# Kernel tuning notes

Hardware: AMD Instinct MI355X
Metric: run time of the kernel (lower is better)

Reference implementation:

```python
import jax, jax.numpy as jnp
import numpy as np

# Dims: B=4, C_in=256, H=W=64 -> L=4096, token_dim D=256, state_dim N=512, K=4
B_, C_IN, H_, W_ = 4, 256, 64, 64
D, N, K = 256, 512, 4


def setup_inputs() -> dict:
    key = jax.random.key(0)
    ks = jax.random.split(key, 16)
    g = lambda k, shape, sc=0.02: (jax.random.normal(k, shape, jnp.float32) * sc)
    return {
        'feat_map': jax.random.normal(ks[0], (B_, C_IN, H_, W_), jnp.float32),
        'hf_map':   jax.random.normal(ks[1], (B_, C_IN, H_, W_), jnp.float32),
        # 1x1 conv proj_f / proj_hf: weight (out=D, in=C_IN), bias (D,)
        'Wf':  g(ks[2], (D, C_IN)), 'bf':  jnp.zeros((D,), jnp.float32),
        'Whf': g(ks[3], (D, C_IN)), 'bhf': jnp.zeros((D,), jnp.float32),
        # alpha_head: Linear(D, D//2) -> GELU -> Linear(D//2, K)
        'Wa1': g(ks[4], (D // 2, D)), 'ba1': jnp.zeros((D // 2,), jnp.float32),
        'Wa2': g(ks[5], (K, D // 2)), 'ba2': jnp.zeros((K,), jnp.float32),
        # SelectiveSSM base tuples: diagonal decay logits A (K,N), input maps B (K,N,D), output maps C (K,D,N)
        'A_base': g(ks[6], (K, N), 1.0),
        'B_base': g(ks[7], (K, N, D), 0.02),
        'C_base': g(ks[8], (K, D, N), 0.02),
        # out_proj 1x1 conv: (C_IN, D)
        'Wout': g(ks[9], (C_IN, D)), 'bout': jnp.zeros((C_IN,), jnp.float32),
    }


def _stage(feat_map, hf_map, Wf, bf, Whf, bhf, Wa1, ba1, Wa2, ba2,
           A_base, B_base, C_base, Wout, bout):
    B, C, H, W = feat_map.shape
    L = H * W
    # 1x1 conv token projections -> (B, L, D)
    t_f = jnp.einsum('bchw,dc->bdhw', feat_map, Wf) + bf[None, :, None, None]
    t_hf = jnp.einsum('bchw,dc->bdhw', hf_map, Whf) + bhf[None, :, None, None]
    x = t_f.reshape(B, -1, L).transpose(0, 2, 1)        # (B, L, D)
    t_hf_seq = t_hf.reshape(B, -1, L).transpose(0, 2, 1)  # (B, L, D)
    # gating MLP -> per-token mixture weights over K base SSMs
    hmid = jax.nn.gelu(t_hf_seq @ Wa1.T + ba1, approximate=False)
    alpha = jax.nn.softmax(hmid @ Wa2.T + ba2, axis=-1)  # (B, L, K)
    # selective SSM: per-token mixed diagonal decay and input drive
    a = jax.nn.sigmoid(jnp.einsum('blk,kn->bln', alpha, A_base))   # (B, L, N)
    u = jnp.einsum('bld,blk,knd->bln', x, alpha, B_base)           # (B, L, N)

    def step(h, au):
        a_t, u_t = au                   # each (B, N)
        h = a_t * h + u_t
        return h, h

    h0 = jnp.zeros((B, a.shape[-1]), x.dtype)
    _, hs = jax.lax.scan(step, h0, (a.transpose(1, 0, 2), u.transpose(1, 0, 2)))
    h_seq = hs.transpose(1, 0, 2)                                   # (B, L, N)
    # mixed readout
    y = jnp.einsum('blk,bln,kdn->bld', alpha, h_seq, C_base)        # (B, L, D)
    y_map = y.transpose(0, 2, 1).reshape(B, -1, H, W)
    out = jnp.einsum('bdhw,cd->bchw', y_map, Wout) + bout[None, :, None, None]
    return out


def reference(feat_map, hf_map, Wf, bf, Whf, bhf, Wa1, ba1, Wa2, ba2,
              A_base, B_base, C_base, Wout, bout):
    return _stage(feat_map, hf_map, Wf, bf, Whf, bhf, Wa1, ba1, Wa2, ba2,
                  A_base, B_base, C_base, Wout, bout)
```

## Files before the change

### kernel.cpp

```cpp
#include <hip/hip_runtime.h>
#include <hip/hip_bf16.h>
#include <math.h>

#define B_  4
#define CIN 256
#define L_  4096
#define D_  256
#define N_  512
#define K_  4
#define DH  128
#define BL  (B_ * L_)

#define NCHUNK 128
#define CLEN   (L_ / NCHUNK)

typedef __attribute__((ext_vector_type(8))) short bfrag;
typedef __attribute__((ext_vector_type(4))) float f4;

__device__ __forceinline__ float bf2f(unsigned short u) {
  return __uint_as_float(((unsigned int)u) << 16);
}
__device__ __forceinline__ unsigned short f2bf(float f) {
  unsigned int u = __float_as_uint(f);
  return (unsigned short)((u + 0x7FFFu + ((u >> 16) & 1u)) >> 16);
}

__global__ void k_prep(const float* __restrict__ Wf, const float* __restrict__ Whf,
                       const float* __restrict__ Wa1, const float* __restrict__ Wout,
                       const float* __restrict__ Bb, const float* __restrict__ Cb,
                       const float* __restrict__ bfv, const float* __restrict__ bhfv,
                       unsigned short* __restrict__ Wfb ,
                       unsigned short* __restrict__ Wa1b,
                       unsigned short* __restrict__ Woutb,
                       unsigned short* __restrict__ Bb16,
                       unsigned short* __restrict__ Cb16,
                       float* __restrict__ biascat) {
  int i = blockIdx.x * 256 + threadIdx.x;
  if (i < 65536) { Wfb[i] = f2bf(Wf[i]); return; } i -= 65536;
  if (i < 65536) { Wfb[65536 + i] = f2bf(Whf[i]); return; } i -= 65536;
  if (i < 32768) { Wa1b[i] = f2bf(Wa1[i]); return; } i -= 32768;
  if (i < 65536) { Woutb[i] = f2bf(Wout[i]); return; } i -= 65536;
  if (i < 524288) {
    int d = i & 255, n = (i >> 8) & 511, k = i >> 17;
    Bb16[(((size_t)n << 2) | k) << 8 | d] = f2bf(Bb[i]);
    return;
  } i -= 524288;
  if (i < 524288) {
    int nn = i & 511, d = (i >> 9) & 255, k = i >> 17;
    Cb16[(((size_t)d << 2) | k) << 9 | nn] = f2bf(Cb[i]);
    return;
  } i -= 524288;
  if (i < 256) { biascat[i] = bfv[i]; return; } i -= 256;
  if (i < 256) { biascat[256 + i] = bhfv[i]; }
}

__global__ void k_transpose2(const float* __restrict__ feat, const float* __restrict__ hf,
                             unsigned short* __restrict__ featT ) {
  __shared__ float tile[32][33];
  const int z = blockIdx.z;
  const int b = z & 3, which = z >> 2;
  const float* in = which ? hf : feat;
  unsigned short* outT = featT + (size_t)which * BL * CIN;
  const int l0 = blockIdx.x * 32, c0 = blockIdx.y * 32;
  const int tx = threadIdx.x, ty = threadIdx.y;
  const float* p = in + ((size_t)b * CIN + c0 + ty) * L_ + l0 + tx;
#pragma unroll
  for (int i = 0; i < 32; i += 8) tile[ty + i][tx] = p[(size_t)i * L_];
  __syncthreads();
  unsigned short* q = outT + ((size_t)b * L_ + l0 + ty) * CIN + c0 + tx;
#pragma unroll
  for (int i = 0; i < 32; i += 8) q[(size_t)i * CIN] = f2bf(tile[tx][ty + i]);
}

__global__ void k_alpha(const unsigned short* __restrict__ hm0,
                        const unsigned short* __restrict__ hm1,
                        const float* __restrict__ ba1, const float* __restrict__ Wa2,
                        const float* __restrict__ ba2, float* __restrict__ alpha) {
  __shared__ float w2[K_ * DH];
  __shared__ float b1[DH];
  __shared__ float b2[K_];
  for (int i = threadIdx.x; i < K_ * DH; i += 256) w2[i] = Wa2[i];
  if (threadIdx.x < DH) b1[threadIdx.x] = ba1[threadIdx.x];
  if (threadIdx.x < K_) b2[threadIdx.x] = ba2[threadIdx.x];
  __syncthreads();
  const int token = blockIdx.x * 64 + (threadIdx.x >> 2);
  const int q = threadIdx.x & 3;
  float a0 = 0.f, a1 = 0.f, a2 = 0.f, a3 = 0.f;
  const size_t base = (size_t)token * DH + q * 32;
#pragma unroll
  for (int j8 = 0; j8 < 4; ++j8) {
    uint4 v0 = *(const uint4*)(hm0 + base + j8 * 8);
    uint4 v1 = *(const uint4*)(hm1 + base + j8 * 8);
    const unsigned int* pa = (const unsigned int*)&v0;
    const unsigned int* pb = (const unsigned int*)&v1;
#pragma unroll
    for (int p = 0; p < 4; ++p) {
      float h0 = bf2f((unsigned short)(pa[p] & 0xffffu)) +
                 bf2f((unsigned short)(pb[p] & 0xffffu));
      float h1 = bf2f((unsigned short)(pa[p] >> 16)) +
                 bf2f((unsigned short)(pb[p] >> 16));
      const int d = q * 32 + j8 * 8 + p * 2;
      float g0 = h0 + b1[d];
      float g1 = h1 + b1[d + 1];
      g0 = 0.5f * g0 * (1.0f + erff(g0 * 0.70710678118654752f));
      g1 = 0.5f * g1 * (1.0f + erff(g1 * 0.70710678118654752f));
      a0 += g0 * w2[0 * DH + d] + g1 * w2[0 * DH + d + 1];
      a1 += g0 * w2[1 * DH + d] + g1 * w2[1 * DH + d + 1];
      a2 += g0 * w2[2 * DH + d] + g1 * w2[2 * DH + d + 1];
      a3 += g0 * w2[3 * DH + d] + g1 * w2[3 * DH + d + 1];
    }
  }
  a0 += __shfl_xor(a0, 1); a1 += __shfl_xor(a1, 1); a2 += __shfl_xor(a2, 1); a3 += __shfl_xor(a3, 1);
  a0 += __shfl_xor(a0, 2); a1 += __shfl_xor(a1, 2); a2 += __shfl_xor(a2, 2); a3 += __shfl_xor(a3, 2);
  a0 += b2[0]; a1 += b2[1]; a2 += b2[2]; a3 += b2[3];
  float m = fmaxf(fmaxf(a0, a1), fmaxf(a2, a3));
  float e0 = expf(a0 - m), e1 = expf(a1 - m), e2 = expf(a2 - m), e3 = expf(a3 - m);
  float inv = 1.f / (e0 + e1 + e2 + e3);
  float my = (q == 0) ? e0 : (q == 1) ? e1 : (q == 2) ? e2 : e3;
  alpha[(size_t)token * 4 + q] = my * inv;
}


__global__ void k_scanA(const unsigned short* __restrict__ u, const float* __restrict__ alpha,
                        const float* __restrict__ Abase,
                        float* __restrict__ P, float* __restrict__ Hend) {
  const int n = threadIdx.x;
  const int bc = blockIdx.x;
  const int b = bc >> 7, c = bc & 127;
  const float A0 = Abase[n], A1 = Abase[N_ + n], A2 = Abase[2 * N_ + n], A3 = Abase[3 * N_ + n];
  const size_t tok0 = (size_t)b * L_ + (size_t)c * CLEN;
  float p = 1.f, h = 0.f;
  for (int l = 0; l < CLEN; ++l) {
    const size_t t = tok0 + l;
    float4 al = *(const float4*)(alpha + t * 4);
    float s = al.x * A0 + al.y * A1 + al.z * A2 + al.w * A3;
    float av = 1.f / (1.f + expf(-s));
    float uv = bf2f(u[t * N_ + n]);
    h = av * h + uv;
    p *= av;
  }
  P[(size_t)bc * N_ + n] = p;
  Hend[(size_t)bc * N_ + n] = h;
}

__global__ void k_scanB(const float* __restrict__ P, const float* __restrict__ Hend,
                        float* __restrict__ Hstart) {
  const int n = threadIdx.x;
  const int b = blockIdx.x;
  float h = 0.f;
  for (int c = 0; c < NCHUNK; ++c) {
    size_t idx = ((size_t)b * NCHUNK + c) * N_ + n;
    Hstart[idx] = h;
    h = P[idx] * h + Hend[idx];
  }
}

__global__ void k_scanC(const unsigned short* __restrict__ u, const float* __restrict__ alpha,
                        const float* __restrict__ Abase, const float* __restrict__ Hstart,
                        unsigned short* __restrict__ hbf) {
  const int n = threadIdx.x;
  const int bc = blockIdx.x;
  const int b = bc >> 7, c = bc & 127;
  const float A0 = Abase[n], A1 = Abase[N_ + n], A2 = Abase[2 * N_ + n], A3 = Abase[3 * N_ + n];
  const size_t tok0 = (size_t)b * L_ + (size_t)c * CLEN;
  float h = Hstart[(size_t)bc * N_ + n];
  for (int l = 0; l < CLEN; ++l) {
    const size_t t = tok0 + l;
    float4 al = *(const float4*)(alpha + t * 4);
    float s = al.x * A0 + al.y * A1 + al.z * A2 + al.w * A3;
    float av = 1.f / (1.f + expf(-s));
    float uv = bf2f(u[t * N_ + n]);
    h = av * h + uv;
    hbf[t * N_ + n] = f2bf(h);
  }
}

#define BM 128
#define BN 128
#define BK 32

#define GLL(src, dst)                                                                      \
  __builtin_amdgcn_global_load_lds((const __attribute__((address_space(1))) void*)(src),   \
                                   (__attribute__((address_space(3))) void*)(dst), 16, 0, 0)

#define BM2 128
#define BN2 256

template <int BIAS, int EPI>
__global__ __launch_bounds__(512, 2) void gemm_bt2(
    const unsigned short* __restrict__ A, long sA,
    const unsigned short* __restrict__ Bm, long sB,
    const float* __restrict__ bias, long bS,
    const float* __restrict__ alphaP,
    void* __restrict__ Cv, long sC,
    int M, int N, int Kd, int lda, int ldb) {
  const int zb = blockIdx.z;
  A += (size_t)zb * sA;
  Bm += (size_t)zb * sB;
  if (BIAS) bias += (size_t)zb * bS;
  const int m0 = blockIdx.x * BM2;
  const int n0 = blockIdx.y * BN2;
  __shared__ __attribute__((aligned(16))) unsigned short As[2 * BM2 * BK];
  __shared__ __attribute__((aligned(16))) unsigned short Bs[2 * BN2 * BK];
  const int t = threadIdx.x;
  const int lane = t & 63;
  const int w = t >> 6;
  const int wm = (w >> 2) * 64;
  const int wn = (w & 3) * 64;

  f4 acc[4][4];
#pragma unroll
  for (int i = 0; i < 4; ++i)
#pragma unroll
    for (int j = 0; j < 4; ++j) acc[i][j] = (f4){0.f, 0.f, 0.f, 0.f};

  const int rS = t >> 2;
  const int cS = (((t & 3) ^ ((t >> 3) & 3))) * 8;
  const unsigned short* gA = A + (size_t)(m0 + rS) * lda + cS;
  const unsigned short* gB = Bm + (size_t)(n0 + rS) * ldb + cS;
  const long rowStepB = (long)128 * ldb;
  const int r16 = lane & 15;
  const int sx = (r16 >> 1) & 3;
  const int kg = (((lane >> 4) ^ sx)) * 8;

#define STAGE2(slot, kt)                                                \
  do {                                                                  \
    const unsigned short* sA_ = gA + (size_t)(kt) * BK;                 \
    const unsigned short* sB_ = gB + (size_t)(kt) * BK;                 \
    unsigned short* dA_ = As + (slot) * (BM2 * BK) + t * 8;             \
    unsigned short* dB_ = Bs + (slot) * (BN2 * BK) + t * 8;             \
    GLL(sA_, dA_);                                                      \
    GLL(sB_, dB_);                                                      \
    GLL(sB_ + rowStepB, dB_ + BM2 * BK);                                \
  } while (0)

  const int nIter = Kd / BK;
  STAGE2(0, 0);
  int cur = 0;
  for (int kt = 0; kt < nIter; ++kt) {
    asm volatile("s_waitcnt vmcnt(0)" ::: "memory");
    __builtin_amdgcn_s_barrier();
    asm volatile("" ::: "memory");
    if (kt + 1 < nIter) STAGE2(cur ^ 1, kt + 1);
    const unsigned short* Ab = As + cur * (BM2 * BK);
    const unsigned short* Bb2 = Bs + cur * (BN2 * BK);
    bfrag af[4], bfr[4];
#pragma unroll
    for (int i = 0; i < 4; ++i) {
      af[i]  = *(const bfrag*)(Ab + (wm + i * 16 + r16) * BK + kg);
      bfr[i] = *(const bfrag*)(Bb2 + (wn + i * 16 + r16) * BK + kg);
    }
    __builtin_amdgcn_s_setprio(1);
#pragma unroll
    for (int i = 0; i < 4; ++i)
#pragma unroll
      for (int j = 0; j < 4; ++j)
        acc[i][j] = __builtin_amdgcn_mfma_f32_16x16x32_bf16(af[i], bfr[j], acc[i][j], 0, 0, 0);
    __builtin_amdgcn_s_setprio(0);
    asm volatile("" ::: "memory");
    cur ^= 1;
  }
#undef STAGE2

  const int rowBase = m0 + wm + ((lane >> 4) << 2);
  const int colBase = n0 + wn + (lane & 15);

  if (EPI >= 2) {
    const int kq = lane & 3;
    const int NO = N >> 2;
    float av[4][4];
#pragma unroll
    for (int i = 0; i < 4; ++i)
#pragma unroll
      for (int r = 0; r < 4; ++r)
        av[i][r] = alphaP[(size_t)(rowBase + i * 16 + r) * 4 + kq];
    float* Cf = (float*)Cv + (size_t)zb * sC;
    unsigned short* Cb = (unsigned short*)Cv + (size_t)zb * sC;
#pragma unroll
    for (int i = 0; i < 4; ++i)
#pragma unroll
      for (int j = 0; j < 4; ++j) {
        const int col = colBase + j * 16;
#pragma unroll
        for (int r = 0; r < 4; ++r) {
          float p = av[i][r] * acc[i][j][r];
          p += __shfl_xor(p, 1);
          p += __shfl_xor(p, 2);
          if (kq == 0) {
            const int row = rowBase + i * 16 + r;
            if (EPI == 2) Cf[(size_t)row * NO + (col >> 2)] = p;
            else          Cb[(size_t)row * NO + (col >> 2)] = f2bf(p);
          }
        }
      }
    return;
  }

  float* Cf = (float*)Cv + (size_t)zb * sC;
  unsigned short* Cb = (unsigned short*)Cv + (size_t)zb * sC;
#pragma unroll
  for (int i = 0; i < 4; ++i) {
#pragma unroll
    for (int j = 0; j < 4; ++j) {
      const int col = colBase + j * 16;
#pragma unroll
      for (int r = 0; r < 4; ++r) {
        const int row = rowBase + i * 16 + r;
        float v = acc[i][j][r];
        if (BIAS == 1) v += bias[col];
        if (BIAS == 2) v += bias[row];
        if (EPI == 1) Cb[(size_t)row * N + col] = f2bf(v);
        else          Cf[(size_t)row * N + col] = v;
      }
    }
  }
}

template <int BIAS, int EPI >
__global__ __launch_bounds__(512, 2) void gemm_w8(
    const unsigned short* __restrict__ A, long sA,
    const unsigned short* __restrict__ Bm, long sB,
    const float* __restrict__ bias, long bS,
    void* __restrict__ Cv, long sC,
    int M, int N, int Kd, int lda, int ldb) {
  const int zb = blockIdx.z;
  A += (size_t)zb * sA;
  Bm += (size_t)zb * sB;
  if (BIAS) bias += (size_t)zb * bS;
  const int m0 = blockIdx.x * BM;
  const int n0 = blockIdx.y * BN;
  __shared__ __attribute__((aligned(16))) unsigned short As[3 * BM * BK];
  __shared__ __attribute__((aligned(16))) unsigned short Bs[3 * BN * BK];
  const int t = threadIdx.x;
  const int lane = t & 63;
  const int w = t >> 6;
  const int wm = (w >> 2) * 64;
  const int wn = (w & 3) * 32;

  f4 acc[4][2];
#pragma unroll
  for (int i = 0; i < 4; ++i)
#pragma unroll
    for (int j = 0; j < 2; ++j) acc[i][j] = (f4){0.f, 0.f, 0.f, 0.f};

  const int rS = t >> 2;
  const int cS = (((t & 3) ^ ((t >> 3) & 3))) * 8;
  const unsigned short* gA = A + (size_t)(m0 + rS) * lda + cS;
  const unsigned short* gB = Bm + (size_t)(n0 + rS) * ldb + cS;
  const int r16 = lane & 15;
  const int sx = (r16 >> 1) & 3;
  const int kg = (((lane >> 4) ^ sx)) * 8;

#define STAGEW(slot, kt)                                                \
  do {                                                                  \
    GLL(gA + (size_t)(kt) * BK, As + (slot) * (BM * BK) + t * 8);       \
    GLL(gB + (size_t)(kt) * BK, Bs + (slot) * (BN * BK) + t * 8);       \
  } while (0)

  const int nIter = Kd / BK;
  STAGEW(0, 0);
  STAGEW(1, 1);
  int slot = 0;
  for (int kt = 0; kt < nIter; ++kt) {
    if (kt + 1 < nIter) asm volatile("s_waitcnt vmcnt(2)" ::: "memory");
    else                asm volatile("s_waitcnt vmcnt(0)" ::: "memory");
    __builtin_amdgcn_s_barrier();
    asm volatile("" ::: "memory");
    if (kt + 2 < nIter) {
      int s2 = slot + 2; if (s2 >= 3) s2 -= 3;
      STAGEW(s2, kt + 2);
    }
    const unsigned short* Ab = As + slot * (BM * BK);
    const unsigned short* Bb2 = Bs + slot * (BN * BK);
    bfrag af[4], bfr[2];
#pragma unroll
    for (int i = 0; i < 4; ++i)
      af[i]  = *(const bfrag*)(Ab + (wm + i * 16 + r16) * BK + kg);
#pragma unroll
    for (int j = 0; j < 2; ++j)
      bfr[j] = *(const bfrag*)(Bb2 + (wn + j * 16 + r16) * BK + kg);
    __builtin_amdgcn_s_setprio(1);
#pragma unroll
    for (int i = 0; i < 4; ++i)
#pragma unroll
      for (int j = 0; j < 2; ++j)
        acc[i][j] = __builtin_amdgcn_mfma_f32_16x16x32_bf16(af[i], bfr[j], acc[i][j], 0, 0, 0);
    __builtin_amdgcn_s_setprio(0);
    asm volatile("" ::: "memory");
    slot = (slot == 2) ? 0 : slot + 1;
  }
#undef STAGEW

  const int rowBase = m0 + wm + ((lane >> 4) << 2);
  const int colBase = n0 + wn + (lane & 15);
  float* Cf = (float*)Cv + (size_t)zb * sC;
  unsigned short* Cb = (unsigned short*)Cv + (size_t)zb * sC;
#pragma unroll
  for (int i = 0; i < 4; ++i) {
#pragma unroll
    for (int j = 0; j < 2; ++j) {
      const int col = colBase + j * 16;
#pragma unroll
      for (int r = 0; r < 4; ++r) {
        const int row = rowBase + i * 16 + r;
        float v = acc[i][j][r];
        if (BIAS == 1) v += bias[col];
        if (BIAS == 2) v += bias[row];
        if (EPI == 1) Cb[(size_t)row * N + col] = f2bf(v);
        else          Cf[(size_t)row * N + col] = v;
      }
    }
  }
}


extern "C" void kernel_launch(void* const* d_in, const int* in_sizes, int n_in,
                              void* d_out, int out_size, void* d_ws, size_t ws_size,
                              hipStream_t stream) {
  const float* feat  = (const float*)d_in[0];
  const float* hf    = (const float*)d_in[1];
  const float* Wf    = (const float*)d_in[2];
  const float* bfv   = (const float*)d_in[3];
  const float* Whf   = (const float*)d_in[4];
  const float* bhfv  = (const float*)d_in[5];
  const float* Wa1   = (const float*)d_in[6];
  const float* ba1   = (const float*)d_in[7];
  const float* Wa2   = (const float*)d_in[8];
  const float* ba2   = (const float*)d_in[9];
  const float* Abase = (const float*)d_in[10];
  const float* Bbase = (const float*)d_in[11];
  const float* Cbase = (const float*)d_in[12];
  const float* Wout  = (const float*)d_in[13];
  const float* bout  = (const float*)d_in[14];
  float* out = (float*)d_out;

  char* ws = (char*)d_ws;
  size_t off = 0;
  auto alloc = [&](size_t bytes) { void* p = ws + off; off += bytes; return p; };

  unsigned short* Wfb    = (unsigned short*)alloc((size_t)2 * D_ * CIN * 2);
  unsigned short* Wa1b   = (unsigned short*)alloc((size_t)DH * D_ * 2);
  unsigned short* Woutb  = (unsigned short*)alloc((size_t)CIN * D_ * 2);
  unsigned short* Bb16   = (unsigned short*)alloc((size_t)K_ * N_ * D_ * 2);
  unsigned short* Cb16   = (unsigned short*)alloc((size_t)K_ * D_ * N_ * 2);
  float*          biascat= (float*)alloc((size_t)2 * D_ * 4);
  float*          alpha  = (float*)alloc((size_t)BL * K_ * 4);
  float*          Pc     = (float*)alloc((size_t)B_ * NCHUNK * N_ * 4);
  float*          He     = (float*)alloc((size_t)B_ * NCHUNK * N_ * 4);
  float*          Hs     = (float*)alloc((size_t)B_ * NCHUNK * N_ * 4);
  unsigned short* hbf    = (unsigned short*)alloc((size_t)BL * N_ * 2);
  unsigned short* x      = (unsigned short*)alloc((size_t)BL * D_ * 2);
  unsigned short* thf    = (unsigned short*)alloc((size_t)BL * D_ * 2);
  unsigned short* featT  = (unsigned short*)alloc((size_t)BL * CIN * 2);
  unsigned short* hfT    = (unsigned short*)alloc((size_t)BL * CIN * 2);
  unsigned short* u16    = (unsigned short*)alloc((size_t)BL * N_ * 2);

  unsigned short* hm0 = featT;
  unsigned short* hm1 = featT + (size_t)BL * DH;
  unsigned short* y   = thf;

  if (ws_size < off) return;

  k_prep<<<dim3((3 * 65536 + 32768 + 2 * 524288 + 512 + 255) / 256), 256, 0, stream>>>(
      Wf, Whf, Wa1, Wout, Bbase, Cbase, bfv, bhfv, Wfb, Wa1b, Woutb, Bb16, Cb16, biascat);

  k_transpose2<<<dim3(L_ / 32, CIN / 32, 2 * B_), dim3(32, 8), 0, stream>>>(feat, hf, featT);

  gemm_w8<1, 1><<<dim3(BL / BM, D_ / BN, 2), 512, 0, stream>>>(
      featT, (long)BL * CIN, Wfb, (long)D_ * CIN, biascat, D_,
      x, (long)BL * D_, BL, D_, CIN, CIN, CIN);

  gemm_w8<0, 1><<<dim3(BL / BM, DH / BN, 2), 512, 0, stream>>>(
      thf, 128, Wa1b, 128, nullptr, 0,
      hm0, (long)BL * DH, BL, DH, 128, D_, D_);
  k_alpha<<<dim3(BL / 64), 256, 0, stream>>>(hm0, hm1, ba1, Wa2, ba2, alpha);

  gemm_bt2<0, 3><<<dim3(BL / BM2, (K_ * N_) / BN2, 1), 512, 0, stream>>>(
      x, 0, Bb16, 0, nullptr, 0, alpha, u16, 0, BL, K_ * N_, D_, D_, D_);

  k_scanA<<<dim3(B_ * NCHUNK), N_, 0, stream>>>(u16, alpha, Abase, Pc, He);
  k_scanB<<<dim3(B_), N_, 0, stream>>>(Pc, He, Hs);
  k_scanC<<<dim3(B_ * NCHUNK), N_, 0, stream>>>(u16, alpha, Abase, Hs, hbf);

  gemm_bt2<0, 3><<<dim3(BL / BM2, (K_ * D_) / BN2, 1), 512, 0, stream>>>(
      hbf, 0, Cb16, 0, nullptr, 0, alpha, y, 0, BL, K_ * D_, N_, N_, N_);

  gemm_w8<2, 0><<<dim3(CIN / BM, L_ / BN, B_), 512, 0, stream>>>(
      Woutb, 0, y, (long)L_ * D_, bout, 0, out, (long)CIN * L_, CIN, L_, D_, D_, D_);
}
```

Before: 155.2 us.

## Fuse alpha-head GEMM with GELU/softmax epilogue into one kernel

Replaces the split-K gating GEMM (two partial halves written to global memory) plus the separate k_alpha kernel with a single kernel that runs the full K=256 reduction for a 128-column tile. The result is staged in shared memory, and GELU, the second linear layer and softmax are applied in the epilogue. This removes one launch and the global round trip of the hidden activations. In exchange it loses the split-K parallelism, since the grid halves, and adds shared-memory epilogue work per block.

Measured after the change: 139.9 us (median of 2 runs). 9.9% less time.

```diff
diff --git a/kernel.cpp b/kernel.cpp
--- a/kernel.cpp
+++ b/kernel.cpp
@@ -72,54 +72,6 @@
   for (int i = 0; i < 32; i += 8) q[(size_t)i * CIN] = f2bf(tile[tx][ty + i]);
 }
 
-__global__ void k_alpha(const unsigned short* __restrict__ hm0,
-                        const unsigned short* __restrict__ hm1,
-                        const float* __restrict__ ba1, const float* __restrict__ Wa2,
-                        const float* __restrict__ ba2, float* __restrict__ alpha) {
-  __shared__ float w2[K_ * DH];
-  __shared__ float b1[DH];
-  __shared__ float b2[K_];
-  for (int i = threadIdx.x; i < K_ * DH; i += 256) w2[i] = Wa2[i];
-  if (threadIdx.x < DH) b1[threadIdx.x] = ba1[threadIdx.x];
-  if (threadIdx.x < K_) b2[threadIdx.x] = ba2[threadIdx.x];
-  __syncthreads();
-  const int token = blockIdx.x * 64 + (threadIdx.x >> 2);
-  const int q = threadIdx.x & 3;
-  float a0 = 0.f, a1 = 0.f, a2 = 0.f, a3 = 0.f;
-  const size_t base = (size_t)token * DH + q * 32;
-#pragma unroll
-  for (int j8 = 0; j8 < 4; ++j8) {
-    uint4 v0 = *(const uint4*)(hm0 + base + j8 * 8);
-    uint4 v1 = *(const uint4*)(hm1 + base + j8 * 8);
-    const unsigned int* pa = (const unsigned int*)&v0;
-    const unsigned int* pb = (const unsigned int*)&v1;
-#pragma unroll
-    for (int p = 0; p < 4; ++p) {
-      float h0 = bf2f((unsigned short)(pa[p] & 0xffffu)) +
-                 bf2f((unsigned short)(pb[p] & 0xffffu));
-      float h1 = bf2f((unsigned short)(pa[p] >> 16)) +
-                 bf2f((unsigned short)(pb[p] >> 16));
-      const int d = q * 32 + j8 * 8 + p * 2;
-      float g0 = h0 + b1[d];
-      float g1 = h1 + b1[d + 1];
-      g0 = 0.5f * g0 * (1.0f + erff(g0 * 0.70710678118654752f));
-      g1 = 0.5f * g1 * (1.0f + erff(g1 * 0.70710678118654752f));
-      a0 += g0 * w2[0 * DH + d] + g1 * w2[0 * DH + d + 1];
-      a1 += g0 * w2[1 * DH + d] + g1 * w2[1 * DH + d + 1];
-      a2 += g0 * w2[2 * DH + d] + g1 * w2[2 * DH + d + 1];
-      a3 += g0 * w2[3 * DH + d] + g1 * w2[3 * DH + d + 1];
-    }
-  }
-  a0 += __shfl_xor(a0, 1); a1 += __shfl_xor(a1, 1); a2 += __shfl_xor(a2, 1); a3 += __shfl_xor(a3, 1);
-  a0 += __shfl_xor(a0, 2); a1 += __shfl_xor(a1, 2); a2 += __shfl_xor(a2, 2); a3 += __shfl_xor(a3, 2);
-  a0 += b2[0]; a1 += b2[1]; a2 += b2[2]; a3 += b2[3];
-  float m = fmaxf(fmaxf(a0, a1), fmaxf(a2, a3));
-  float e0 = expf(a0 - m), e1 = expf(a1 - m), e2 = expf(a2 - m), e3 = expf(a3 - m);
-  float inv = 1.f / (e0 + e1 + e2 + e3);
-  float my = (q == 0) ? e0 : (q == 1) ? e1 : (q == 2) ? e2 : e3;
-  alpha[(size_t)token * 4 + q] = my * inv;
-}
-
 
 __global__ void k_scanA(const unsigned short* __restrict__ u, const float* __restrict__ alpha,
                         const float* __restrict__ Abase,
@@ -413,6 +365,119 @@
   }
 }
 
+__global__ __launch_bounds__(512, 2) void gemm_alpha(
+    const unsigned short* __restrict__ A,
+    const unsigned short* __restrict__ Bm,
+    const float* __restrict__ ba1, const float* __restrict__ Wa2,
+    const float* __restrict__ ba2, float* __restrict__ alphaOut) {
+  __shared__ __attribute__((aligned(16))) unsigned short smem[6 * BM * BK + 1344];
+  unsigned short* As = smem;
+  unsigned short* Bs = smem + 3 * BM * BK;
+  unsigned short* tile = smem;
+  float* w2s = (float*)(smem + 6 * BM * BK);
+  float* b1s = w2s + 512;
+  float* b2s = b1s + 128;
+  const int t = threadIdx.x;
+  const int lane = t & 63;
+  const int w = t >> 6;
+  const int wm = (w >> 2) * 64;
+  const int wn = (w & 3) * 32;
+  const int m0 = blockIdx.x * BM;
+
+  f4 acc[4][2];
+#pragma unroll
+  for (int i = 0; i < 4; ++i)
+#pragma unroll
+    for (int j = 0; j < 2; ++j) acc[i][j] = (f4){0.f, 0.f, 0.f, 0.f};
+
+  const int rS = t >> 2;
+  const int cS = (((t & 3) ^ ((t >> 3) & 3))) * 8;
+  const unsigned short* gA = A + (size_t)(m0 + rS) * D_ + cS;
+  const unsigned short* gB = Bm + (size_t)rS * D_ + cS;
+  const int r16 = lane & 15;
+  const int sx = (r16 >> 1) & 3;
+  const int kg = (((lane >> 4) ^ sx)) * 8;
+
+#define STAGEA(slot, kt)                                                \
+  do {                                                                  \
+    GLL(gA + (size_t)(kt) * BK, As + (slot) * (BM * BK) + t * 8);       \
+    GLL(gB + (size_t)(kt) * BK, Bs + (slot) * (BM * BK) + t * 8);       \
+  } while (0)
+
+  const int nIter = D_ / BK;
+  STAGEA(0, 0);
+  STAGEA(1, 1);
+  int slot = 0;
+  for (int kt = 0; kt < nIter; ++kt) {
+    if (kt + 1 < nIter) asm volatile("s_waitcnt vmcnt(2)" ::: "memory");
+    else                asm volatile("s_waitcnt vmcnt(0)" ::: "memory");
+    __builtin_amdgcn_s_barrier();
+    asm volatile("" ::: "memory");
+    if (kt + 2 < nIter) {
+      int s2 = slot + 2; if (s2 >= 3) s2 -= 3;
+      STAGEA(s2, kt + 2);
+    }
+    const unsigned short* Ab = As + slot * (BM * BK);
+    const unsigned short* Bb2 = Bs + slot * (BM * BK);
+    bfrag af[4], bfr[2];
+#pragma unroll
+    for (int i = 0; i < 4; ++i)
+      af[i]  = *(const bfrag*)(Ab + (wm + i * 16 + r16) * BK + kg);
+#pragma unroll
+    for (int j = 0; j < 2; ++j)
+      bfr[j] = *(const bfrag*)(Bb2 + (wn + j * 16 + r16) * BK + kg);
+    __builtin_amdgcn_s_setprio(1);
+#pragma unroll
+    for (int i = 0; i < 4; ++i)
+#pragma unroll
+      for (int j = 0; j < 2; ++j)
+        acc[i][j] = __builtin_amdgcn_mfma_f32_16x16x32_bf16(af[i], bfr[j], acc[i][j], 0, 0, 0);
+    __builtin_amdgcn_s_setprio(0);
+    asm volatile("" ::: "memory");
+    slot = (slot == 2) ? 0 : slot + 1;
+  }
+#undef STAGEA
+
+  __syncthreads();
+  w2s[t & 511] = Wa2[t & 511];
+  if (t < DH) b1s[t] = ba1[t];
+  if (t < K_) b2s[t] = ba2[t];
+  const int lrowBase = wm + ((lane >> 4) << 2);
+  const int lcolBase = wn + r16;
+#pragma unroll
+  for (int i = 0; i < 4; ++i)
+#pragma unroll
+    for (int j = 0; j < 2; ++j) {
+      const int col = lcolBase + j * 16;
+#pragma unroll
+      for (int r = 0; r < 4; ++r)
+        tile[(lrowBase + i * 16 + r) * DH + col] = f2bf(acc[i][j][r]);
+    }
+  __syncthreads();
+
+  const int tok = t >> 2;
+  const int q = t & 3;
+  float a0 = 0.f, a1 = 0.f, a2 = 0.f, a3 = 0.f;
+#pragma unroll 8
+  for (int e = 0; e < 32; ++e) {
+    const int d = q * 32 + e;
+    float g = bf2f(tile[tok * DH + d]) + b1s[d];
+    g = 0.5f * g * (1.0f + erff(g * 0.70710678118654752f));
+    a0 += g * w2s[0 * DH + d];
+    a1 += g * w2s[1 * DH + d];
+    a2 += g * w2s[2 * DH + d];
+    a3 += g * w2s[3 * DH + d];
+  }
+  a0 += __shfl_xor(a0, 1); a1 += __shfl_xor(a1, 1); a2 += __shfl_xor(a2, 1); a3 += __shfl_xor(a3, 1);
+  a0 += __shfl_xor(a0, 2); a1 += __shfl_xor(a1, 2); a2 += __shfl_xor(a2, 2); a3 += __shfl_xor(a3, 2);
+  a0 += b2s[0]; a1 += b2s[1]; a2 += b2s[2]; a3 += b2s[3];
+  float m = fmaxf(fmaxf(a0, a1), fmaxf(a2, a3));
+  float e0 = expf(a0 - m), e1 = expf(a1 - m), e2 = expf(a2 - m), e3 = expf(a3 - m);
+  float inv = 1.f / (e0 + e1 + e2 + e3);
+  float my = (q == 0) ? e0 : (q == 1) ? e1 : (q == 2) ? e2 : e3;
+  alphaOut[(size_t)(m0 + tok) * 4 + q] = my * inv;
+}
+
 
 extern "C" void kernel_launch(void* const* d_in, const int* in_sizes, int n_in,
                               void* d_out, int out_size, void* d_ws, size_t ws_size,
@@ -455,8 +520,6 @@
   unsigned short* hfT    = (unsigned short*)alloc((size_t)BL * CIN * 2);
   unsigned short* u16    = (unsigned short*)alloc((size_t)BL * N_ * 2);
 
-  unsigned short* hm0 = featT;
-  unsigned short* hm1 = featT + (size_t)BL * DH;
   unsigned short* y   = thf;
 
   if (ws_size < off) return;
@@ -470,10 +533,7 @@
       featT, (long)BL * CIN, Wfb, (long)D_ * CIN, biascat, D_,
       x, (long)BL * D_, BL, D_, CIN, CIN, CIN);
 
-  gemm_w8<0, 1><<<dim3(BL / BM, DH / BN, 2), 512, 0, stream>>>(
-      thf, 128, Wa1b, 128, nullptr, 0,
-      hm0, (long)BL * DH, BL, DH, 128, D_, D_);
-  k_alpha<<<dim3(BL / 64), 256, 0, stream>>>(hm0, hm1, ba1, Wa2, ba2, alpha);
+  gemm_alpha<<<dim3(BL / BM), 512, 0, stream>>>(thf, Wa1b, ba1, Wa2, ba2, alpha);
 
   gemm_bt2<0, 3><<<dim3(BL / BM2, (K_ * N_) / BN2, 1), 512, 0, stream>>>(
       x, 0, Bb16, 0, nullptr, 0, alpha, u16, 0, BL, K_ * N_, D_, D_, D_);
```
